# Kernel tuning notes

Measured on AMD Instinct MI355X. Metric: run time of the kernel, lower is better.

## Reference

```python
import jax, jax.numpy as jnp
import numpy as np

N_HEAD = 16
N_KV_HEAD = 4
HEAD_DIM = 64  # n_embd // n_head = 1024 // 16
N_EMBD = 1024


def _alibi_bias(T, n_head, head_dim):
    # slopes: start = 2**(-2**(-(log2(H)-3))); slope_i = start**(i+1)
    start = 2.0 ** (-2.0 ** (-(np.log2(n_head) - 3.0)))
    slopes = jnp.asarray(start ** np.arange(1, n_head + 1), dtype=jnp.float32)  # [H]
    rel = (jnp.arange(T, dtype=jnp.float32)[None, :]
           - jnp.arange(T, dtype=jnp.float32)[:, None])  # [T,T], rel[i,j] = j - i
    bias = slopes[:, None, None] * rel[None, :, :]  # [H,T,T]
    # Faithful to the torch module: masked_fill(-inf) is then OVERWRITTEN by
    # torch.tril, which zeroes the upper triangle. Net effect: lower-tri alibi
    # values, 0 above the diagonal (NO causal masking).
    bias = jnp.tril(bias)
    return bias * (head_dim ** -0.5)  # extra scale applied in forward


def setup_inputs() -> dict:
    key = jax.random.key(0)
    ks = jax.random.split(key, 5)
    B, T, C = 4, 2048, N_EMBD
    w_scale = 0.02
    return {
        "x": jax.random.normal(ks[0], (B, T, C), dtype=jnp.float32),
        "Wq": jax.random.normal(ks[1], (C, C), dtype=jnp.float32) * w_scale,
        "Wkv": jax.random.normal(ks[2], (2 * N_KV_HEAD * HEAD_DIM, C), dtype=jnp.float32) * w_scale,
        "Wproj": jax.random.normal(ks[3], (C, C), dtype=jnp.float32) * w_scale,
        "bproj": jnp.zeros((C,), dtype=jnp.float32),
    }


def reference(x, Wq, Wkv, Wproj, bproj):
    B, T, C = x.shape
    H, KVH, D = N_HEAD, N_KV_HEAD, HEAD_DIM
    ratio = H // KVH

    q = jnp.einsum('btc,ec->bte', x, Wq).reshape(B, T, H, D).transpose(0, 2, 1, 3)  # [B,H,T,D]
    kv = jnp.einsum('btc,ec->bte', x, Wkv)  # [B,T,2*KVH*D]
    k, v = jnp.split(kv, 2, axis=-1)
    k = k.reshape(B, T, KVH, D).transpose(0, 2, 1, 3)  # [B,KVH,T,D]
    v = v.reshape(B, T, KVH, D).transpose(0, 2, 1, 3)
    # torch .repeat tiles whole blocks: query head h uses kv head h % KVH
    k = jnp.tile(k, (1, ratio, 1, 1))  # [B,H,T,D]
    v = jnp.tile(v, (1, ratio, 1, 1))

    bias = _alibi_bias(T, H, D)  # [H,T,T], already *= D**-0.5
    scores = jnp.einsum('bhtd,bhsd->bhts', q, k) * (D ** -0.5) + bias[None]
    attn = jax.nn.softmax(scores, axis=-1)
    out = jnp.einsum('bhts,bhsd->bhtd', attn, v)  # [B,H,T,D]
    out = out.transpose(0, 2, 1, 3).reshape(B, T, C)
    return jnp.einsum('btc,ec->bte', out, Wproj) + bproj
```

## Files before the change

kernel.cpp:

```cpp
#include <hip/hip_runtime.h>
#include <hip/hip_bf16.h>
#include <cstdint>

typedef __bf16 bf16;
typedef bf16 bf16x2 __attribute__((ext_vector_type(2)));
typedef bf16 bf16x4 __attribute__((ext_vector_type(4)));
typedef bf16 bf16x8 __attribute__((ext_vector_type(8)));
typedef float f32x4 __attribute__((ext_vector_type(4)));

#define MFMA16(a, b, c) __builtin_amdgcn_mfma_f32_16x16x32_bf16((a), (b), (c), 0, 0, 0)

#define QSCALE 0.18033688011112042f

__device__ inline void async16(const bf16* g, bf16* l) {
  __builtin_amdgcn_global_load_lds(
      (const __attribute__((address_space(1))) void*)g,
      (__attribute__((address_space(3))) void*)l, 16, 0, 0);
}

__global__ void cast_f32_to_bf16(const float* __restrict__ src,
                                 bf16* __restrict__ dst, int n4) {
  int i = blockIdx.x * blockDim.x + threadIdx.x;
  if (i < n4) {
    const float4 v = ((const float4*)src)[i];
    bf16x4 o;
    o.x = (bf16)v.x; o.y = (bf16)v.y; o.z = (bf16)v.z; o.w = (bf16)v.w;
    ((bf16x4*)dst)[i] = o;
  }
}

__global__ __launch_bounds__(256, 2)
void gemm_qkv(const bf16* __restrict__ A, const bf16* __restrict__ B,
              bf16* __restrict__ qb, bf16* __restrict__ kb, bf16* __restrict__ vb) {
  constexpr int K = 1024;
  __shared__ bf16 sA[128 * 64];
  __shared__ bf16 sB[128 * 64];
  const int tid = threadIdx.x;
  const int lane = tid & 63, wid = tid >> 6;
  const int col = lane & 15, quad = lane >> 4;
  const int wm = wid >> 1, wn = wid & 1;
  const int m0 = blockIdx.y * 128, n0 = blockIdx.x * 128;
  const int c7 = col & 7;

  f32x4 acc[4][4];
  const f32x4 z = {0.f, 0.f, 0.f, 0.f};
#pragma unroll
  for (int mi = 0; mi < 4; mi++)
#pragma unroll
    for (int ni = 0; ni < 4; ni++) acc[mi][ni] = z;

  for (int k0 = 0; k0 < K; k0 += 64) {
    __syncthreads();
#pragma unroll
    for (int c = 0; c < 4; ++c) {
      const int idx = c * 256 + tid;
      const int row = idx >> 3, kc = idx & 7;
      const int gkc = kc ^ (row & 7);
      async16(&A[(size_t)(m0 + row) * K + k0 + gkc * 8], &sA[idx * 8]);
      async16(&B[(size_t)(n0 + row) * K + k0 + gkc * 8], &sB[idx * 8]);
    }
    __syncthreads();
#pragma unroll
    for (int ks = 0; ks < 2; ++ks) {
      bf16x8 af[4], bfr[4];
#pragma unroll
      for (int i = 0; i < 4; i++)
        af[i] = *(const bf16x8*)&sA[(wm * 64 + i * 16 + col) * 64 +
                                    (((ks * 4 + quad) ^ c7) << 3)];
#pragma unroll
      for (int i = 0; i < 4; i++)
        bfr[i] = *(const bf16x8*)&sB[(wn * 64 + i * 16 + col) * 64 +
                                     (((ks * 4 + quad) ^ c7) << 3)];
#pragma unroll
      for (int mi = 0; mi < 4; mi++)
#pragma unroll
        for (int ni = 0; ni < 4; ni++)
          acc[mi][ni] = MFMA16(af[mi], bfr[ni], acc[mi][ni]);
    }
  }
#pragma unroll
  for (int mi = 0; mi < 4; mi++) {
#pragma unroll
    for (int ni = 0; ni < 4; ni++) {
      const int e = n0 + wn * 64 + ni * 16 + col;
#pragma unroll
      for (int r = 0; r < 4; r++) {
        const int m = m0 + wm * 64 + mi * 16 + quad * 4 + r;
        const int bb = m >> 11, t = m & 2047;
        if (e < 1024) {
          qb[(((size_t)bb * 16 + (e >> 6)) * 2048 + t) * 64 + (e & 63)] =
              (bf16)(acc[mi][ni][r] * QSCALE);
        } else if (e < 1280) {
          const int f = e - 1024;
          kb[(((size_t)bb * 4 + (f >> 6)) * 2048 + t) * 64 + (f & 63)] =
              (bf16)acc[mi][ni][r];
        } else {
          const int f = e - 1280;
          vb[(((size_t)bb * 4 + (f >> 6)) * 2048 + t) * 64 + (f & 63)] =
              (bf16)acc[mi][ni][r];
        }
      }
    }
  }
}

__global__ __launch_bounds__(256, 2)
void gemm_proj(const bf16* __restrict__ A, const bf16* __restrict__ B,
               const float* __restrict__ bias, float* __restrict__ out) {
  constexpr int K = 1024;
  __shared__ bf16 sA[128 * 64];
  __shared__ bf16 sB[128 * 64];
  const int tid = threadIdx.x;
  const int lane = tid & 63, wid = tid >> 6;
  const int col = lane & 15, quad = lane >> 4;
  const int wm = wid >> 1, wn = wid & 1;
  const int m0 = blockIdx.y * 128, n0 = blockIdx.x * 128;
  const int c7 = col & 7;

  f32x4 acc[4][4];
  const f32x4 z = {0.f, 0.f, 0.f, 0.f};
#pragma unroll
  for (int mi = 0; mi < 4; mi++)
#pragma unroll
    for (int ni = 0; ni < 4; ni++) acc[mi][ni] = z;

  for (int k0 = 0; k0 < K; k0 += 64) {
    __syncthreads();
#pragma unroll
    for (int c = 0; c < 4; ++c) {
      const int idx = c * 256 + tid;
      const int row = idx >> 3, kc = idx & 7;
      const int gkc = kc ^ (row & 7);
      async16(&A[(size_t)(m0 + row) * K + k0 + gkc * 8], &sA[idx * 8]);
      async16(&B[(size_t)(n0 + row) * K + k0 + gkc * 8], &sB[idx * 8]);
    }
    __syncthreads();
#pragma unroll
    for (int ks = 0; ks < 2; ++ks) {
      bf16x8 af[4], bfr[4];
#pragma unroll
      for (int i = 0; i < 4; i++)
        af[i] = *(const bf16x8*)&sA[(wm * 64 + i * 16 + col) * 64 +
                                    (((ks * 4 + quad) ^ c7) << 3)];
#pragma unroll
      for (int i = 0; i < 4; i++)
        bfr[i] = *(const bf16x8*)&sB[(wn * 64 + i * 16 + col) * 64 +
                                     (((ks * 4 + quad) ^ c7) << 3)];
#pragma unroll
      for (int mi = 0; mi < 4; mi++)
#pragma unroll
        for (int ni = 0; ni < 4; ni++)
          acc[mi][ni] = MFMA16(af[mi], bfr[ni], acc[mi][ni]);
    }
  }
#pragma unroll
  for (int mi = 0; mi < 4; mi++) {
#pragma unroll
    for (int ni = 0; ni < 4; ni++) {
      const int e = n0 + wn * 64 + ni * 16 + col;
      const float be = bias[e];
#pragma unroll
      for (int r = 0; r < 4; r++) {
        const int m = m0 + wm * 64 + mi * 16 + quad * 4 + r;
        out[(size_t)m * 1024 + e] = acc[mi][ni][r] + be;
      }
    }
  }
}

__global__ __launch_bounds__(256, 2)
void attn_alibi(const bf16* __restrict__ qb, const bf16* __restrict__ kb,
                const bf16* __restrict__ vb, bf16* __restrict__ ob) {
  __shared__ bf16 sK[64 * 64];
  __shared__ bf16 sVt[64 * 72];
  __shared__ bf16 sPt[4][64 * 64];
  const int tid = threadIdx.x;
  const int lane = tid & 63, wid = tid >> 6;
  const int col = lane & 15, quad = lane >> 4;
  const int c7 = col & 7;
  const int bh = blockIdx.y;
  const int b = bh >> 4, h = bh & 15, kvh = h & 3;
  const int qbase = __builtin_amdgcn_readfirstlane(blockIdx.x * 256 + wid * 64);

  const bf16* qptr = qb + ((size_t)(b * 16 + h) * 2048 + qbase) * 64;
  const bf16* kptr = kb + ((size_t)(b * 4 + kvh) * 2048) * 64;
  const bf16* vptr = vb + ((size_t)(b * 4 + kvh) * 2048) * 64;

  bf16x8 bq[4][2];
#pragma unroll
  for (int ni = 0; ni < 4; ni++)
#pragma unroll
    for (int ks = 0; ks < 2; ks++)
      bq[ni][ks] = *(const bf16x8*)&qptr[(ni * 16 + col) * 64 + ks * 32 + quad * 8];

  bf16x8 bones;
#pragma unroll
  for (int j = 0; j < 8; j++) bones[j] = (bf16)1.0f;

  f32x4 O[4][4];
  f32x4 Osum[4];
  const f32x4 z = {0.f, 0.f, 0.f, 0.f};
#pragma unroll
  for (int mi = 0; mi < 4; mi++) {
    Osum[mi] = z;
#pragma unroll
    for (int nd = 0; nd < 4; nd++) O[mi][nd] = z;
  }

  const float cb = exp2f(-0.5f * (float)(h + 1)) * QSCALE;
  const int qoff = quad * 4 - col;

  const int rk0 = tid >> 3, rk1 = 32 + rk0, kc = tid & 7;
  const int rv = rk0 * 2;
  const int blkv = rv >> 3, rlv = rv & 7;
  const int kx = (kc ^ (rk0 & 7)) << 3;

  bf16x8 kr0 = *(const bf16x8*)&kptr[(size_t)rk0 * 64 + kc * 8];
  bf16x8 kr1 = *(const bf16x8*)&kptr[(size_t)rk1 * 64 + kc * 8];
  bf16x8 vr0 = *(const bf16x8*)&vptr[(size_t)rv * 64 + kc * 8];
  bf16x8 vr1 = *(const bf16x8*)&vptr[(size_t)(rv + 1) * 64 + kc * 8];

  for (int c0 = 0; c0 < 2048; c0 += 64) {
    __syncthreads();
    *(bf16x8*)&sK[rk0 * 64 + kx] = kr0;
    *(bf16x8*)&sK[rk1 * 64 + kx] = kr1;
#pragma unroll
    for (int j = 0; j < 8; j++) {
      bf16x2 pr;
      pr.x = vr0[j];
      pr.y = vr1[j];
      *(bf16x2*)&sVt[(kc * 8 + j) * 72 + ((blkv ^ kc) << 3) + rlv] = pr;
    }
    __syncthreads();

    {
      const int cn = (c0 + 64 < 2048) ? c0 + 64 : 0;
      kr0 = *(const bf16x8*)&kptr[(size_t)(cn + rk0) * 64 + kc * 8];
      kr1 = *(const bf16x8*)&kptr[(size_t)(cn + rk1) * 64 + kc * 8];
      vr0 = *(const bf16x8*)&vptr[(size_t)(cn + rv) * 64 + kc * 8];
      vr1 = *(const bf16x8*)&vptr[(size_t)(cn + rv + 1) * 64 + kc * 8];
    }

    f32x4 S[4][4];
#pragma unroll
    for (int mi = 0; mi < 4; mi++)
#pragma unroll
      for (int ni = 0; ni < 4; ni++) S[mi][ni] = z;
#pragma unroll
    for (int ks = 0; ks < 2; ks++) {
      bf16x8 ak[4];
#pragma unroll
      for (int mi = 0; mi < 4; mi++)
        ak[mi] = *(const bf16x8*)&sK[(mi * 16 + col) * 64 +
                                     (((ks * 4 + quad) ^ c7) << 3)];
#pragma unroll
      for (int mi = 0; mi < 4; mi++)
#pragma unroll
        for (int ni = 0; ni < 4; ni++)
          S[mi][ni] = MFMA16(ak[mi], bq[ni][ks], S[mi][ni]);
    }

    bf16* sp = sPt[wid];
#pragma unroll
    for (int ni = 0; ni < 4; ni++) {
#pragma unroll
      for (int mi = 0; mi < 4; mi++) {
        const int U = c0 + mi * 16 - qbase - ni * 16;
        f32x4 p;
        if (U <= -15) {
          const float bb = cb * (float)(U + qoff);
#pragma unroll
          for (int r = 0; r < 4; r++)
            p[r] = __builtin_amdgcn_exp2f(S[mi][ni][r] + (bb + cb * (float)r));
        } else if (U >= 16) {
#pragma unroll
          for (int r = 0; r < 4; r++)
            p[r] = __builtin_amdgcn_exp2f(S[mi][ni][r]);
        } else {
          const float relf = (float)(U + qoff);
#pragma unroll
          for (int r = 0; r < 4; r++) {
            const float rr = relf + (float)r;
            const float bb = (rr <= 0.f) ? cb * rr : 0.f;
            p[r] = __builtin_amdgcn_exp2f(S[mi][ni][r] + bb);
          }
        }
        bf16x4 w;
#pragma unroll
        for (int r = 0; r < 4; r++) w[r] = (bf16)p[r];
        *(bf16x4*)&sp[(ni * 16 + col) * 64 +
                      (((2 * mi + (quad >> 1)) ^ c7) << 3) + ((quad & 1) << 2)] = w;
      }
    }

#pragma unroll
    for (int ks = 0; ks < 2; ks++) {
      bf16x8 ap[4], bv[4];
#pragma unroll
      for (int mi = 0; mi < 4; mi++)
        ap[mi] = *(const bf16x8*)&sp[(mi * 16 + col) * 64 +
                                     (((ks * 4 + quad) ^ c7) << 3)];
#pragma unroll
      for (int nd = 0; nd < 4; nd++) {
        const int d = nd * 16 + col;
        bv[nd] = *(const bf16x8*)&sVt[d * 72 + (((ks * 4 + quad) ^ (d >> 3)) << 3)];
      }
#pragma unroll
      for (int mi = 0; mi < 4; mi++) {
#pragma unroll
        for (int nd = 0; nd < 4; nd++)
          O[mi][nd] = MFMA16(ap[mi], bv[nd], O[mi][nd]);
        Osum[mi] = MFMA16(ap[mi], bones, Osum[mi]);
      }
    }
  }

#pragma unroll
  for (int mi = 0; mi < 4; mi++) {
#pragma unroll
    for (int r = 0; r < 4; r++) {
      const float inv = 1.0f / Osum[mi][r];
      const int t = qbase + mi * 16 + quad * 4 + r;
#pragma unroll
      for (int nd = 0; nd < 4; nd++) {
        ob[((size_t)b * 2048 + t) * 1024 + h * 64 + nd * 16 + col] =
            (bf16)(O[mi][nd][r] * inv);
      }
    }
  }
}

extern "C" void kernel_launch(void* const* d_in, const int* in_sizes, int n_in,
                              void* d_out, int out_size, void* d_ws, size_t ws_size,
                              hipStream_t stream) {
  const float* x     = (const float*)d_in[0];
  const float* Wq    = (const float*)d_in[1];
  const float* Wkv   = (const float*)d_in[2];
  const float* Wproj = (const float*)d_in[3];
  const float* bproj = (const float*)d_in[4];
  float* out = (float*)d_out;

  bf16* xb  = (bf16*)d_ws;
  bf16* w1b = xb  + 8388608;
  bf16* wpb = w1b + 1572864;
  bf16* qb  = wpb + 1048576;
  bf16* kb  = qb  + 8388608;
  bf16* vb  = kb  + 2097152;
  bf16* aob = vb  + 2097152;

  cast_f32_to_bf16<<<8192, 256, 0, stream>>>(x, xb, 2097152);
  cast_f32_to_bf16<<<1024, 256, 0, stream>>>(Wq, w1b, 262144);
  cast_f32_to_bf16<<<512, 256, 0, stream>>>(Wkv, w1b + 1048576, 131072);
  cast_f32_to_bf16<<<1024, 256, 0, stream>>>(Wproj, wpb, 262144);

  gemm_qkv<<<dim3(12, 64), 256, 0, stream>>>(xb, w1b, qb, kb, vb);
  attn_alibi<<<dim3(8, 64), 256, 0, stream>>>(qb, kb, vb, aob);
  gemm_proj<<<dim3(8, 64), 256, 0, stream>>>(aob, wpb, bproj, out);
}
```

Measured before the change: 248.5 us.

## Fuse four cast launches into one and double-buffer attention K/V tiles

```diff
diff --git a/kernel.cpp b/kernel.cpp
--- a/kernel.cpp
+++ b/kernel.cpp
@@ -18,15 +18,27 @@
       (__attribute__((address_space(3))) void*)l, 16, 0, 0);
 }
 
-__global__ void cast_f32_to_bf16(const float* __restrict__ src,
-                                 bf16* __restrict__ dst, int n4) {
-  int i = blockIdx.x * blockDim.x + threadIdx.x;
-  if (i < n4) {
-    const float4 v = ((const float4*)src)[i];
-    bf16x4 o;
-    o.x = (bf16)v.x; o.y = (bf16)v.y; o.z = (bf16)v.z; o.w = (bf16)v.w;
-    ((bf16x4*)dst)[i] = o;
-  }
+__global__ void cast_all(const float* __restrict__ x, const float* __restrict__ wq,
+                         const float* __restrict__ wkv, const float* __restrict__ wp,
+                         bf16* __restrict__ xb, bf16* __restrict__ w1b,
+                         bf16* __restrict__ wpb) {
+  const int i = blockIdx.x * blockDim.x + threadIdx.x;
+  const float4* src;
+  bf16x4* dst;
+  int idx;
+  if (i < 2097152) {
+    src = (const float4*)x; dst = (bf16x4*)xb; idx = i;
+  } else if (i < 2359296) {
+    src = (const float4*)wq; dst = (bf16x4*)w1b; idx = i - 2097152;
+  } else if (i < 2490368) {
+    src = (const float4*)wkv; dst = (bf16x4*)(w1b + 1048576); idx = i - 2359296;
+  } else {
+    src = (const float4*)wp; dst = (bf16x4*)wpb; idx = i - 2490368;
+  }
+  const float4 v = src[idx];
+  bf16x4 o;
+  o.x = (bf16)v.x; o.y = (bf16)v.y; o.z = (bf16)v.z; o.w = (bf16)v.w;
+  dst[idx] = o;
 }
 
 __global__ __launch_bounds__(256, 2)
@@ -171,8 +183,8 @@
 __global__ __launch_bounds__(256, 2)
 void attn_alibi(const bf16* __restrict__ qb, const bf16* __restrict__ kb,
                 const bf16* __restrict__ vb, bf16* __restrict__ ob) {
-  __shared__ bf16 sK[64 * 64];
-  __shared__ bf16 sVt[64 * 72];
+  __shared__ bf16 sK[2][64 * 64];
+  __shared__ bf16 sVt[2][64 * 72];
   __shared__ bf16 sPt[4][64 * 64];
   const int tid = threadIdx.x;
   const int lane = tid & 63, wid = tid >> 6;
@@ -220,16 +232,18 @@
   bf16x8 vr0 = *(const bf16x8*)&vptr[(size_t)rv * 64 + kc * 8];
   bf16x8 vr1 = *(const bf16x8*)&vptr[(size_t)(rv + 1) * 64 + kc * 8];
 
-  for (int c0 = 0; c0 < 2048; c0 += 64) {
-    __syncthreads();
-    *(bf16x8*)&sK[rk0 * 64 + kx] = kr0;
-    *(bf16x8*)&sK[rk1 * 64 + kx] = kr1;
+  int bufi = 0;
+  for (int c0 = 0; c0 < 2048; c0 += 64, bufi ^= 1) {
+    bf16* skw = sK[bufi];
+    bf16* svw = sVt[bufi];
+    *(bf16x8*)&skw[rk0 * 64 + kx] = kr0;
+    *(bf16x8*)&skw[rk1 * 64 + kx] = kr1;
 #pragma unroll
     for (int j = 0; j < 8; j++) {
       bf16x2 pr;
       pr.x = vr0[j];
       pr.y = vr1[j];
-      *(bf16x2*)&sVt[(kc * 8 + j) * 72 + ((blkv ^ kc) << 3) + rlv] = pr;
+      *(bf16x2*)&svw[(kc * 8 + j) * 72 + ((blkv ^ kc) << 3) + rlv] = pr;
     }
     __syncthreads();
 
@@ -251,8 +265,8 @@
       bf16x8 ak[4];
 #pragma unroll
       for (int mi = 0; mi < 4; mi++)
-        ak[mi] = *(const bf16x8*)&sK[(mi * 16 + col) * 64 +
-                                     (((ks * 4 + quad) ^ c7) << 3)];
+        ak[mi] = *(const bf16x8*)&skw[(mi * 16 + col) * 64 +
+                                      (((ks * 4 + quad) ^ c7) << 3)];
 #pragma unroll
       for (int mi = 0; mi < 4; mi++)
 #pragma unroll
@@ -303,7 +317,7 @@
 #pragma unroll
       for (int nd = 0; nd < 4; nd++) {
         const int d = nd * 16 + col;
-        bv[nd] = *(const bf16x8*)&sVt[d * 72 + (((ks * 4 + quad) ^ (d >> 3)) << 3)];
+        bv[nd] = *(const bf16x8*)&svw[d * 72 + (((ks * 4 + quad) ^ (d >> 3)) << 3)];
       }
 #pragma unroll
       for (int mi = 0; mi < 4; mi++) {
@@ -348,11 +362,7 @@
   bf16* vb  = kb  + 2097152;
   bf16* aob = vb  + 2097152;
 
-  cast_f32_to_bf16<<<8192, 256, 0, stream>>>(x, xb, 2097152);
-  cast_f32_to_bf16<<<1024, 256, 0, stream>>>(Wq, w1b, 262144);
-  cast_f32_to_bf16<<<512, 256, 0, stream>>>(Wkv, w1b + 1048576, 131072);
-  cast_f32_to_bf16<<<1024, 256, 0, stream>>>(Wproj, wpb, 262144);
-
+  cast_all<<<10752, 256, 0, stream>>>(x, Wq, Wkv, Wproj, xb, w1b, wpb);
   gemm_qkv<<<dim3(12, 64), 256, 0, stream>>>(xb, w1b, qb, kb, vb);
   attn_alibi<<<dim3(8, 64), 256, 0, stream>>>(qb, kb, vb, aob);
   gemm_proj<<<dim3(8, 64), 256, 0, stream>>>(aob, wpb, bproj, out);
```

Result: faster. 240.4 us (-3.3%).
